# Kernel tuning notes

Measured on AMD Instinct MI355X. Metric: run time of the kernel, lower is better.

The kernel has to match this reference:

```python
import jax, jax.numpy as jnp
import numpy as np

P, RES_H, RES_W = 32, 256, 256
H, W = 480, 640
FOCAL = 1.0


def setup_inputs() -> dict:
    key = jax.random.key(0)
    k1, k2, k3, k4 = jax.random.split(key, 4)
    # texture: alpha + rgb logits, uniform(-1,1) as in torch init
    plane_content = jax.random.uniform(k1, (P, 4, RES_H, RES_W), jnp.float32, -1.0, 1.0)
    # orthonormal plane basis (columns = plane x/y axes + normal)
    plane_basis, _ = jnp.linalg.qr(jax.random.normal(k2, (P, 3, 3), jnp.float32))
    xy = jax.random.normal(k3, (P, 2), jnp.float32)
    z = 2.0 + 4.0 * jax.random.uniform(k4, (P, 1), jnp.float32)  # planes in front of camera
    plane_position = jnp.concatenate([xy, z], axis=-1)
    plane_wh = jnp.full((P, 2), 2.0, jnp.float32)
    cam_R = jnp.eye(3, dtype=jnp.float32)   # world-to-cam rotation
    cam_T = jnp.zeros((3,), jnp.float32)    # world-to-cam translation
    return {"plane_content": plane_content, "plane_basis": plane_basis,
            "plane_position": plane_position, "plane_wh": plane_wh,
            "cam_R": cam_R, "cam_T": cam_T}


def _bilinear(img, uv):
    # img: (C, Hc, Wc); uv: (N, 2) in [-1, 1]. torch grid_sample bilinear,
    # align_corners=False, padding_mode='zeros'.
    C, Hc, Wc = img.shape
    x = (uv[:, 0] + 1.0) * Wc * 0.5 - 0.5
    y = (uv[:, 1] + 1.0) * Hc * 0.5 - 0.5
    x0 = jnp.floor(x)
    y0 = jnp.floor(y)
    wx = x - x0
    wy = y - y0

    def gather(xi, yi):
        inb = (xi >= 0) & (xi < Wc) & (yi >= 0) & (yi < Hc)
        xc = jnp.clip(xi, 0, Wc - 1).astype(jnp.int32)
        yc = jnp.clip(yi, 0, Hc - 1).astype(jnp.int32)
        return jnp.where(inb[None, :], img[:, yc, xc], 0.0)  # (C, N)

    v00 = gather(x0, y0)
    v01 = gather(x0 + 1.0, y0)
    v10 = gather(x0, y0 + 1.0)
    v11 = gather(x0 + 1.0, y0 + 1.0)
    top = v00 * (1.0 - wx) + v01 * wx
    bot = v10 * (1.0 - wx) + v11 * wx
    return (top * (1.0 - wy) + bot * wy).T  # (N, C)


def reference(plane_content, plane_basis, plane_position, plane_wh, cam_R, cam_T):
    N = H * W
    xs = ((jnp.arange(W, dtype=jnp.float32) + 0.5) / W) * 2.0 - 1.0
    ys = ((jnp.arange(H, dtype=jnp.float32) + 0.5) / H) * 2.0 - 1.0
    gy, gx = jnp.meshgrid(ys, xs, indexing='ij')
    # pinhole ray directions in camera frame (z-depth parameterization)
    dirs_cam = jnp.stack([gx.reshape(-1) / FOCAL, gy.reshape(-1) / FOCAL,
                          jnp.ones((N,), jnp.float32)], axis=-1)  # (N,3)
    cam_pos = -cam_R.T @ cam_T                 # camera center in world
    dirs_world = dirs_cam @ cam_R              # R^T d per ray, (N,3)

    normals = plane_basis[:, :, 2]             # (P,3)
    num = jnp.einsum('pc,pc->p', normals, plane_position - cam_pos[None])
    den = jnp.einsum('pc,nc->pn', normals, dirs_world)
    den = jnp.where(jnp.abs(den) < 1e-6, 1e-6, den)
    points_depth = num[:, None] / den          # (P,N) depth on each plane

    world_points = cam_pos[None, None] + points_depth[..., None] * dirs_world[None]  # (P,N,3)
    local = jnp.einsum('pnc,pcd->pnd', world_points - plane_position[:, None], plane_basis)
    uv = local[..., :2] / (plane_wh[:, None, :] * 0.5)        # normalize to [-1,1] inside plane
    in_planes = jnp.all(jnp.abs(uv) <= 1.0, axis=-1)          # (P,N)

    raw = jax.vmap(_bilinear)(plane_content, uv)              # (P,N,4)
    content = jnp.where(in_planes[..., None], jax.nn.sigmoid(raw), 0.0)

    sort_idx = jnp.argsort(points_depth, axis=0)              # front-to-back per pixel
    depth_sorted = jnp.take_along_axis(points_depth, sort_idx, axis=0)
    content_sorted = jnp.take_along_axis(content, sort_idx[..., None], axis=0)

    alpha = content_sorted[..., 0]                            # (P,N)
    color = content_sorted[..., 1:]                           # (P,N,3)
    trans = jnp.cumprod(1.0 - alpha, axis=0)
    trans = jnp.concatenate([jnp.ones((1, N), alpha.dtype), trans[:-1]], axis=0)
    weight = alpha * trans                                    # (P,N)

    depth_img = jnp.sum(depth_sorted * weight, axis=0).reshape(H, W)
    color_img = jnp.sum(color * weight[..., None], axis=0).reshape(H, W, 3)
    return jnp.concatenate([color_img, depth_img[..., None]], axis=-1)  # (H,W,4)
```

## Files before the change

kernel.cpp:

```cpp
#include <hip/hip_runtime.h>
#include <cstdint>

constexpr int P   = 32;
constexpr int RES = 256;
constexpr int H   = 480;
constexpr int W   = 640;
#define KMAX 0xFFFFFFFFu

__device__ __forceinline__ uint32_t mono_key(float f) {
    uint32_t b = __float_as_uint(f);
    return (b & 0x80000000u) ? ~b : (b | 0x80000000u);
}
__device__ __forceinline__ float unmono(uint32_t m) {
    uint32_t b = (m & 0x80000000u) ? (m ^ 0x80000000u) : ~m;
    return __uint_as_float(b);
}
__device__ __forceinline__ float h2f(unsigned short u) {
    return (float)__builtin_bit_cast(_Float16, u);
}
__device__ __forceinline__ unsigned short f2h(float f) {
    return __builtin_bit_cast(unsigned short, (_Float16)f);
}

__global__ __launch_bounds__(256) void prep_repack_kernel(
    const float* __restrict__ content,
    const float* __restrict__ basis, const float* __restrict__ ppos,
    const float* __restrict__ pwh,   const float* __restrict__ camR,
    const float* __restrict__ camT,
    float4* __restrict__ tab, ushort4* __restrict__ tex)
{
    const int tid = blockIdx.x * 256 + threadIdx.x;
    const float* src = content + (((size_t)(tid >> 16)) << 18) + (tid & 65535);
    ushort4 o;
    o.x = f2h(src[0]);
    o.y = f2h(src[65536]);
    o.z = f2h(src[131072]);
    o.w = f2h(src[196608]);
    tex[tid] = o;

    if (blockIdx.x == 0 && threadIdx.x < P) {
        const int p = threadIdx.x;
        const float R0=camR[0],R1=camR[1],R2=camR[2],
                    R3=camR[3],R4=camR[4],R5=camR[5],
                    R6=camR[6],R7=camR[7],R8=camR[8];
        (void)R1;(void)R2;(void)R4;(void)R5;(void)R7;(void)R8;
        const float T0=camT[0],T1=camT[1],T2=camT[2];
        const float cpx = -(camR[0]*T0 + camR[3]*T1 + camR[6]*T2);
        const float cpy = -(camR[1]*T0 + camR[4]*T1 + camR[7]*T2);
        const float cpz = -(camR[2]*T0 + camR[5]*T1 + camR[8]*T2);
        (void)R0;(void)R3;(void)R6;
        const float* b = basis + 9 * p;
        const float n0 = b[2], n1 = b[5], n2 = b[8];
        const float px = ppos[3*p], py = ppos[3*p+1], pz = ppos[3*p+2];
        const float num = n0*(px-cpx) + n1*(py-cpy) + n2*(pz-cpz);
        const float A0  = (cpx-px)*b[0] + (cpy-py)*b[3] + (cpz-pz)*b[6];
        const float A1  = (cpx-px)*b[1] + (cpy-py)*b[4] + (cpz-pz)*b[7];
        const float hw0 = pwh[2*p]   * 0.5f;
        const float hw1 = pwh[2*p+1] * 0.5f;
        tab[4*p+0] = make_float4(n0, n1, n2, num);
        tab[4*p+1] = make_float4(A0, A1, __int_as_float(p << 16), 0.f);
        tab[4*p+2] = make_float4(b[0], b[3], b[6], 1.0f/hw0);
        tab[4*p+3] = make_float4(b[1], b[4], b[7], 1.0f/hw1);
    }
}

__global__ __launch_bounds__(256, 4) void render_fast(
    const ushort4* __restrict__ tex, const float4* __restrict__ tab,
    const float* __restrict__ camR,  float* __restrict__ out)
{
    __shared__ float4 s_pl[P][5];

    const int t = threadIdx.x;
    if (t < P) {
        s_pl[t][0] = tab[4*t+1];
        s_pl[t][1] = tab[4*t+2];
        s_pl[t][2] = tab[4*t+3];
    }
    __syncthreads();

    const int x = blockIdx.x * 16 + (t & 15);
    const int y = blockIdx.y * 16 + (t >> 4);
    const float gx = ((float)x + 0.5f) / (float)W * 2.0f - 1.0f;
    const float gy = ((float)y + 0.5f) / (float)H * 2.0f - 1.0f;
    const float dwx = gx*camR[0] + gy*camR[3] + camR[6];
    const float dwy = gx*camR[1] + gy*camR[4] + camR[7];
    const float dwz = gx*camR[2] + gy*camR[5] + camR[8];

    uint32_t key[P];
    #pragma unroll
    for (int p = 0; p < P; ++p) {
        const float4 c0 = tab[4*p+0];
        const float4 c1 = tab[4*p+1];
        const float4 c2 = tab[4*p+2];
        const float4 c3 = tab[4*p+3];
        float den = c0.x*dwx + c0.y*dwy + c0.z*dwz;
        if (fabsf(den) < 1e-6f) den = 1e-6f;
        const float d  = c0.w / den;
        const float B0 = c2.x*dwx + c2.y*dwy + c2.z*dwz;
        const float B1 = c3.x*dwx + c3.y*dwy + c3.z*dwz;
        const float u  = (c1.x + d*B0) * c2.w;
        const float v  = (c1.y + d*B1) * c3.w;
        key[p] = (fabsf(u) <= 1.0f && fabsf(v) <= 1.0f) ? mono_key(d) : KMAX;
    }

    float aR = 0.f, aG = 0.f, aB = 0.f, aD = 0.f, tr = 1.f;

    auto argmin_pop = [&](int& obi) -> uint32_t {
        uint32_t bk = KMAX; int bi = 0;
        #pragma unroll
        for (int i = 0; i < P; ++i) {
            const bool c = key[i] < bk;
            bk = c ? key[i] : bk;
            bi = c ? i : bi;
        }
        #pragma unroll
        for (int i = 0; i < P; ++i)
            key[i] = (i == bi) ? KMAX : key[i];
        obi = bi;
        return bk;
    };

    struct St { ushort4 t00, t01, t10, t11; float d, wx, wy; int ix, iy; bool valid; };

    auto issue = [&](uint32_t k, int bi) -> St {
        St s;
        s.valid = (k != KMAX);
        const float d = s.valid ? unmono(k) : 0.0f;
        const float4 pA = s_pl[bi][0];
        const float4 pB = s_pl[bi][1];
        const float4 pC = s_pl[bi][2];
        const float B0 = pB.x*dwx + pB.y*dwy + pB.z*dwz;
        const float B1 = pC.x*dwx + pC.y*dwy + pC.z*dwz;
        const float u  = (pA.x + d*B0) * pB.w;
        const float v  = (pA.y + d*B1) * pC.w;
        const float fx = (u + 1.0f) * 128.0f - 0.5f;
        const float fy = (v + 1.0f) * 128.0f - 0.5f;
        const float x0f = floorf(fx), y0f = floorf(fy);
        s.wx = fx - x0f; s.wy = fy - y0f;
        s.ix = (int)x0f; s.iy = (int)y0f;
        s.d = d;
        const int x0c = min(max(s.ix,     0), RES-1);
        const int x1c = min(max(s.ix + 1, 0), RES-1);
        const int y0c = min(max(s.iy,     0), RES-1);
        const int y1c = min(max(s.iy + 1, 0), RES-1);
        const int base = __float_as_int(pA.z);
        const int r0 = base + (y0c << 8), r1 = base + (y1c << 8);
        s.t00 = tex[r0 + x0c]; s.t01 = tex[r0 + x1c];
        s.t10 = tex[r1 + x0c]; s.t11 = tex[r1 + x1c];
        return s;
    };

    auto consume = [&](const St& s) {
        ushort4 t00 = s.t00, t01 = s.t01, t10 = s.t10, t11 = s.t11;
        const bool mx0 = (uint32_t)s.ix       < (uint32_t)RES;
        const bool mx1 = (uint32_t)(s.ix + 1) < (uint32_t)RES;
        const bool my0 = (uint32_t)s.iy       < (uint32_t)RES;
        const bool my1 = (uint32_t)(s.iy + 1) < (uint32_t)RES;
        if (!(mx0 && my0)) { t00.x = t00.y = t00.z = t00.w = 0; }
        if (!(mx1 && my0)) { t01.x = t01.y = t01.z = t01.w = 0; }
        if (!(mx0 && my1)) { t10.x = t10.y = t10.z = t10.w = 0; }
        if (!(mx1 && my1)) { t11.x = t11.y = t11.z = t11.w = 0; }
        const float omwx = 1.0f - s.wx, omwy = 1.0f - s.wy;
        const unsigned short* q00 = (const unsigned short*)&t00;
        const unsigned short* q01 = (const unsigned short*)&t01;
        const unsigned short* q10 = (const unsigned short*)&t10;
        const unsigned short* q11 = (const unsigned short*)&t11;
        float c4[4];
        #pragma unroll
        for (int c = 0; c < 4; ++c) {
            const float top = h2f(q00[c]) * omwx + h2f(q01[c]) * s.wx;
            const float bot = h2f(q10[c]) * omwx + h2f(q11[c]) * s.wx;
            const float raw = top * omwy + bot * s.wy;
            c4[c] = __builtin_amdgcn_rcpf(1.0f + __expf(-raw));
        }
        const float a   = s.valid ? c4[0] : 0.0f;
        const float wgt = a * tr;
        aD += s.d * wgt;
        aR += c4[1] * wgt;
        aG += c4[2] * wgt;
        aB += c4[3] * wgt;
        tr *= (1.0f - a);
    };

    int cbi; uint32_t ck = argmin_pop(cbi);
    if (__ballot(ck != KMAX) != 0ull) {
        St cur = issue(ck, cbi);
        for (;;) {
            int nbi; const uint32_t nk = argmin_pop(nbi);
            const bool more = (__ballot(nk != KMAX) != 0ull);
            St nxt;
            if (more) nxt = issue(nk, nbi);
            consume(cur);
            if (!more) break;
            cur = nxt;
        }
    }

    const int o = (y * W + x) * 4;
    float4 res; res.x = aR; res.y = aG; res.z = aB; res.w = aD;
    *reinterpret_cast<float4*>(out + o) = res;
}

__global__ __launch_bounds__(256) void render_ref(
    const float* __restrict__ content, const float* __restrict__ basis,
    const float* __restrict__ ppos,    const float* __restrict__ pwh,
    const float* __restrict__ camR,    const float* __restrict__ camT,
    float* __restrict__ out)
{
    __shared__ float s_pl[P][20];
    const int t = threadIdx.x;
    const int x = blockIdx.x * 16 + (t & 15);
    const int y = blockIdx.y * 16 + (t >> 4);
    if (t < P) {
        const float* b = basis + t * 9;
        s_pl[t][0] = b[0]; s_pl[t][1] = b[3]; s_pl[t][2] = b[6];
        s_pl[t][3] = b[1]; s_pl[t][4] = b[4]; s_pl[t][5] = b[7];
        s_pl[t][6] = ppos[t*3+0]; s_pl[t][7] = ppos[t*3+1]; s_pl[t][8] = ppos[t*3+2];
        s_pl[t][9] = pwh[t*2+0] * 0.5f; s_pl[t][10] = pwh[t*2+1] * 0.5f;
    }
    __syncthreads();
    const float T0=camT[0],T1=camT[1],T2=camT[2];
    const float cpx = -(camR[0]*T0 + camR[3]*T1 + camR[6]*T2);
    const float cpy = -(camR[1]*T0 + camR[4]*T1 + camR[7]*T2);
    const float cpz = -(camR[2]*T0 + camR[5]*T1 + camR[8]*T2);
    const float gx = ((float)x + 0.5f) / (float)W * 2.0f - 1.0f;
    const float gy = ((float)y + 0.5f) / (float)H * 2.0f - 1.0f;
    const float dwx = gx*camR[0] + gy*camR[3] + camR[6];
    const float dwy = gx*camR[1] + gy*camR[4] + camR[7];
    const float dwz = gx*camR[2] + gy*camR[5] + camR[8];
    uint32_t key[P];
    #pragma unroll
    for (int p = 0; p < P; ++p) {
        const float b00=basis[p*9+0], b01=basis[p*9+1], n0=basis[p*9+2];
        const float b10=basis[p*9+3], b11=basis[p*9+4], n1=basis[p*9+5];
        const float b20=basis[p*9+6], b21=basis[p*9+7], n2=basis[p*9+8];
        const float px=ppos[p*3+0], py=ppos[p*3+1], pz=ppos[p*3+2];
        const float hw0=pwh[p*2+0]*0.5f, hw1=pwh[p*2+1]*0.5f;
        const float num = n0*(px-cpx) + n1*(py-cpy) + n2*(pz-cpz);
        float den = n0*dwx + n1*dwy + n2*dwz;
        if (fabsf(den) < 1e-6f) den = 1e-6f;
        const float depth = num / den;
        const float ox = cpx + depth*dwx - px;
        const float oy = cpy + depth*dwy - py;
        const float oz = cpz + depth*dwz - pz;
        const float u = (ox*b00 + oy*b10 + oz*b20) / hw0;
        const float v = (ox*b01 + oy*b11 + oz*b21) / hw1;
        key[p] = (fabsf(u) <= 1.0f && fabsf(v) <= 1.0f) ? mono_key(depth) : KMAX;
    }
    float aR=0.f,aG=0.f,aB=0.f,aD=0.f,tr=1.f;
    #pragma unroll 1
    for (int it = 0; it < P; ++it) {
        uint32_t bk = KMAX; int bi = 0;
        #pragma unroll
        for (int i = 0; i < P; ++i) {
            const bool c = key[i] < bk;
            bk = c ? key[i] : bk; bi = c ? i : bi;
        }
        if (bk == KMAX) break;
        #pragma unroll
        for (int i = 0; i < P; ++i) key[i] = (i == bi) ? KMAX : key[i];
        const float depth = unmono(bk);
        const float* pl = s_pl[bi];
        const float ox = cpx + depth*dwx - pl[6];
        const float oy = cpy + depth*dwy - pl[7];
        const float oz = cpz + depth*dwz - pl[8];
        const float u = (ox*pl[0] + oy*pl[1] + oz*pl[2]) / pl[9];
        const float v = (ox*pl[3] + oy*pl[4] + oz*pl[5]) / pl[10];
        const float fx = (u + 1.0f) * 128.0f - 0.5f;
        const float fy = (v + 1.0f) * 128.0f - 0.5f;
        const float x0f = floorf(fx), y0f = floorf(fy);
        const float wx = fx - x0f, wy = fy - y0f;
        const int ix = (int)x0f, iy = (int)y0f;
        const int x0c = min(max(ix,0),RES-1), x1c = min(max(ix+1,0),RES-1);
        const int y0c = min(max(iy,0),RES-1), y1c = min(max(iy+1,0),RES-1);
        const float m00 = ((uint32_t)ix<(uint32_t)RES && (uint32_t)iy<(uint32_t)RES) ? 1.f:0.f;
        const float m01 = ((uint32_t)(ix+1)<(uint32_t)RES && (uint32_t)iy<(uint32_t)RES) ? 1.f:0.f;
        const float m10 = ((uint32_t)ix<(uint32_t)RES && (uint32_t)(iy+1)<(uint32_t)RES) ? 1.f:0.f;
        const float m11 = ((uint32_t)(ix+1)<(uint32_t)RES && (uint32_t)(iy+1)<(uint32_t)RES) ? 1.f:0.f;
        const int o00=y0c*RES+x0c, o01=y0c*RES+x1c, o10=y1c*RES+x0c, o11=y1c*RES+x1c;
        const float* pc = content + ((size_t)bi << 18);
        float c4[4];
        #pragma unroll
        for (int c = 0; c < 4; ++c) {
            const float* ic = pc + (c << 16);
            const float v00 = ic[o00]*m00, v01 = ic[o01]*m01;
            const float v10 = ic[o10]*m10, v11 = ic[o11]*m11;
            const float top = v00*(1.f-wx) + v01*wx;
            const float bot = v10*(1.f-wx) + v11*wx;
            const float raw = top*(1.f-wy) + bot*wy;
            c4[c] = 1.0f / (1.0f + __expf(-raw));
        }
        const float wgt = c4[0]*tr;
        aD += depth*wgt; aR += c4[1]*wgt; aG += c4[2]*wgt; aB += c4[3]*wgt;
        tr *= (1.0f - c4[0]);
    }
    const int o = (y * W + x) * 4;
    float4 res; res.x=aR; res.y=aG; res.z=aB; res.w=aD;
    *reinterpret_cast<float4*>(out + o) = res;
}

extern "C" void kernel_launch(void* const* d_in, const int* in_sizes, int n_in,
                              void* d_out, int out_size, void* d_ws, size_t ws_size,
                              hipStream_t stream) {
    const float* content = (const float*)d_in[0];
    const float* basis   = (const float*)d_in[1];
    const float* ppos    = (const float*)d_in[2];
    const float* pwh     = (const float*)d_in[3];
    const float* camR    = (const float*)d_in[4];
    const float* camT    = (const float*)d_in[5];

    dim3 grid(W / 16, H / 16);
    const size_t TAB_BYTES = 2048;
    const size_t need = TAB_BYTES + (size_t)P * 65536 * sizeof(ushort4);

    if (ws_size >= need) {
        float4*  tab = (float4*)d_ws;
        ushort4* tex = (ushort4*)((char*)d_ws + TAB_BYTES);
        prep_repack_kernel<<<P * 65536 / 256, 256, 0, stream>>>(
            content, basis, ppos, pwh, camR, camT, tab, tex);
        render_fast<<<grid, dim3(256), 0, stream>>>(tex, tab, camR, (float*)d_out);
    } else {
        render_ref<<<grid, dim3(256), 0, stream>>>(
            content, basis, ppos, pwh, camR, camT, (float*)d_out);
    }
}
```

Measured before the change: 37.16 us.

## Deepen texture-fetch pipeline to four stages, remap tiles, and early-exit empty waves

The render loop now keeps four outstanding bilinear texture fetches in flight instead of one. Its trip count comes from a wave-wide maximum of per-pixel hit counts, replacing a ballot taken on every iteration. Blocks use a 1-D grid with a swizzled block-to-tile mapping, presumably to spread spatially adjacent tiles across XCDs. Waves with no hits write zeros and exit early. Invalid fetches are clamped to index zero, and the occupancy hint drops from 4 to 2 to leave room for the extra registers, which risks lower latency hiding.

```diff
diff --git a/kernel.cpp b/kernel.cpp
--- a/kernel.cpp
+++ b/kernel.cpp
@@ -40,15 +40,10 @@
 
     if (blockIdx.x == 0 && threadIdx.x < P) {
         const int p = threadIdx.x;
-        const float R0=camR[0],R1=camR[1],R2=camR[2],
-                    R3=camR[3],R4=camR[4],R5=camR[5],
-                    R6=camR[6],R7=camR[7],R8=camR[8];
-        (void)R1;(void)R2;(void)R4;(void)R5;(void)R7;(void)R8;
         const float T0=camT[0],T1=camT[1],T2=camT[2];
         const float cpx = -(camR[0]*T0 + camR[3]*T1 + camR[6]*T2);
         const float cpy = -(camR[1]*T0 + camR[4]*T1 + camR[7]*T2);
         const float cpz = -(camR[2]*T0 + camR[5]*T1 + camR[8]*T2);
-        (void)R0;(void)R3;(void)R6;
         const float* b = basis + 9 * p;
         const float n0 = b[2], n1 = b[5], n2 = b[8];
         const float px = ppos[3*p], py = ppos[3*p+1], pz = ppos[3*p+2];
@@ -64,11 +59,11 @@
     }
 }
 
-__global__ __launch_bounds__(256, 4) void render_fast(
+__global__ __launch_bounds__(256, 2) void render_fast(
     const ushort4* __restrict__ tex, const float4* __restrict__ tab,
     const float* __restrict__ camR,  float* __restrict__ out)
 {
-    __shared__ float4 s_pl[P][5];
+    __shared__ float4 s_pl[P][3];
 
     const int t = threadIdx.x;
     if (t < P) {
@@ -78,8 +73,12 @@
     }
     __syncthreads();
 
-    const int x = blockIdx.x * 16 + (t & 15);
-    const int y = blockIdx.y * 16 + (t >> 4);
+    const int orig = blockIdx.x;
+    const int s_id = (orig >> 3) + (orig & 7) * 150;
+    const int tx = s_id % 40, ty = s_id / 40;
+    const int x = tx * 16 + (t & 15);
+    const int y = ty * 16 + (t >> 4);
+
     const float gx = ((float)x + 0.5f) / (float)W * 2.0f - 1.0f;
     const float gy = ((float)y + 0.5f) / (float)H * 2.0f - 1.0f;
     const float dwx = gx*camR[0] + gy*camR[3] + camR[6];
@@ -87,6 +86,7 @@
     const float dwz = gx*camR[2] + gy*camR[5] + camR[8];
 
     uint32_t key[P];
+    int cnt = 0;
     #pragma unroll
     for (int p = 0; p < P; ++p) {
         const float4 c0 = tab[4*p+0];
@@ -100,7 +100,21 @@
         const float B1 = c3.x*dwx + c3.y*dwy + c3.z*dwz;
         const float u  = (c1.x + d*B0) * c2.w;
         const float v  = (c1.y + d*B1) * c3.w;
-        key[p] = (fabsf(u) <= 1.0f && fabsf(v) <= 1.0f) ? mono_key(d) : KMAX;
+        const bool hit = (fabsf(u) <= 1.0f && fabsf(v) <= 1.0f);
+        key[p] = hit ? mono_key(d) : KMAX;
+        cnt += hit ? 1 : 0;
+    }
+
+    int wmax = cnt;
+    #pragma unroll
+    for (int off = 32; off; off >>= 1)
+        wmax = max(wmax, __shfl_xor(wmax, off));
+
+    const int o = (y * W + x) * 4;
+    if (wmax == 0) {
+        float4 z; z.x = z.y = z.z = z.w = 0.f;
+        *reinterpret_cast<float4*>(out + o) = z;
+        return;
     }
 
     float aR = 0.f, aG = 0.f, aB = 0.f, aD = 0.f, tr = 1.f;
@@ -139,11 +153,12 @@
         s.wx = fx - x0f; s.wy = fy - y0f;
         s.ix = (int)x0f; s.iy = (int)y0f;
         s.d = d;
-        const int x0c = min(max(s.ix,     0), RES-1);
-        const int x1c = min(max(s.ix + 1, 0), RES-1);
-        const int y0c = min(max(s.iy,     0), RES-1);
-        const int y1c = min(max(s.iy + 1, 0), RES-1);
-        const int base = __float_as_int(pA.z);
+        int x0c = min(max(s.ix,     0), RES-1);
+        int x1c = min(max(s.ix + 1, 0), RES-1);
+        int y0c = min(max(s.iy,     0), RES-1);
+        int y1c = min(max(s.iy + 1, 0), RES-1);
+        int base = __float_as_int(pA.z);
+        if (!s.valid) { base = 0; x0c = x1c = y0c = y1c = 0; }
         const int r0 = base + (y0c << 8), r1 = base + (y1c << 8);
         s.t00 = tex[r0 + x0c]; s.t01 = tex[r0 + x1c];
         s.t10 = tex[r1 + x0c]; s.t11 = tex[r1 + x1c];
@@ -182,21 +197,35 @@
         tr *= (1.0f - a);
     };
 
-    int cbi; uint32_t ck = argmin_pop(cbi);
-    if (__ballot(ck != KMAX) != 0ull) {
-        St cur = issue(ck, cbi);
-        for (;;) {
-            int nbi; const uint32_t nk = argmin_pop(nbi);
-            const bool more = (__ballot(nk != KMAX) != 0ull);
-            St nxt;
-            if (more) nxt = issue(nk, nbi);
-            consume(cur);
-            if (!more) break;
-            cur = nxt;
-        }
-    }
-
-    const int o = (y * W + x) * 4;
+    int b0, b1, b2, b3;
+    uint32_t k0 = argmin_pop(b0);
+    uint32_t k1 = argmin_pop(b1);
+    uint32_t k2 = argmin_pop(b2);
+    uint32_t k3 = argmin_pop(b3);
+    St s0 = issue(k0, b0);
+    St s1 = issue(k1, b1);
+    St s2 = issue(k2, b2);
+    St s3 = issue(k3, b3);
+
+    int rem = wmax;
+    for (;;) {
+        const int left = rem - 4;
+        consume(s0);
+        s0.valid = false;
+        if (left > 0) { k0 = argmin_pop(b0); s0 = issue(k0, b0); }
+        consume(s1);
+        s1.valid = false;
+        if (left > 1) { k1 = argmin_pop(b1); s1 = issue(k1, b1); }
+        consume(s2);
+        s2.valid = false;
+        if (left > 2) { k2 = argmin_pop(b2); s2 = issue(k2, b2); }
+        consume(s3);
+        s3.valid = false;
+        if (left > 3) { k3 = argmin_pop(b3); s3 = issue(k3, b3); }
+        rem = left;
+        if (left <= 0) break;
+    }
+
     float4 res; res.x = aR; res.y = aG; res.z = aB; res.w = aD;
     *reinterpret_cast<float4*>(out + o) = res;
 }
@@ -309,7 +338,6 @@
     const float* camR    = (const float*)d_in[4];
     const float* camT    = (const float*)d_in[5];
 
-    dim3 grid(W / 16, H / 16);
     const size_t TAB_BYTES = 2048;
     const size_t need = TAB_BYTES + (size_t)P * 65536 * sizeof(ushort4);
 
@@ -318,8 +346,10 @@
         ushort4* tex = (ushort4*)((char*)d_ws + TAB_BYTES);
         prep_repack_kernel<<<P * 65536 / 256, 256, 0, stream>>>(
             content, basis, ppos, pwh, camR, camT, tab, tex);
-        render_fast<<<grid, dim3(256), 0, stream>>>(tex, tab, camR, (float*)d_out);
+        render_fast<<<dim3(1200), dim3(256), 0, stream>>>(
+            tex, tab, camR, (float*)d_out);
     } else {
+        dim3 grid(W / 16, H / 16);
         render_ref<<<grid, dim3(256), 0, stream>>>(
             content, basis, ppos, pwh, camR, camT, (float*)d_out);
     }
```

Measured after the change: 49.12 us. +32.2%, slower.
